# Kernel optimization log

Hardware: AMD Instinct MI355X
Metric: run time of the kernel (lower is better)

## Reference

```python
import jax, jax.numpy as jnp
import numpy as np

DIM = 1024
QKV_DIM = 64      # per-head dim
NUM_HEADS = 16
NUM_TOKENS = 1024
BATCH = 8
SCALE = QKV_DIM ** (-0.5)


def setup_inputs() -> dict:
    key = jax.random.key(0)
    k1, k2, k3 = jax.random.split(key, 3)
    x = jax.random.normal(k1, (BATCH, NUM_TOKENS, DIM), dtype=jnp.float32)
    # qkv Linear (no bias): dim -> 3 * num_heads * qkv_dim
    W_qkv = jax.random.normal(k2, (DIM, 3 * NUM_HEADS * QKV_DIM), dtype=jnp.float32) * (DIM ** -0.5)
    # reg parameter initialized to ones / num_tokens (as in nn.Parameter init)
    reg = jnp.ones((1, NUM_HEADS, NUM_TOKENS, NUM_TOKENS), dtype=jnp.float32) / NUM_TOKENS
    W_proj = jax.random.normal(k3, (NUM_HEADS * QKV_DIM, DIM), dtype=jnp.float32) * ((NUM_HEADS * QKV_DIM) ** -0.5)
    b_proj = jnp.zeros((DIM,), dtype=jnp.float32)
    return {"x": x, "W_qkv": W_qkv, "reg": reg, "W_proj": W_proj, "b_proj": b_proj}


def reference(x, W_qkv, reg, W_proj, b_proj) -> jnp.ndarray:
    B, N, C = x.shape
    H, D = NUM_HEADS, QKV_DIM
    qkv = (x @ W_qkv).reshape(B, N, 3, H, D)          # [B,N,3,H,D]
    qkv = jnp.transpose(qkv, (2, 0, 3, 1, 4))         # [3,B,H,N,D]
    q, k, v = qkv[0], qkv[1], qkv[2]
    attn = jnp.einsum('bhnd,bhmd->bhnm', q, k) * SCALE  # [B,H,N,N]
    attn = jax.nn.softmax(attn, axis=-1)
    attn = attn + reg                                   # post-softmax learned bias (broadcast over batch)
    # dropout p=0.0 -> identity
    out = jnp.einsum('bhnm,bhmd->bhnd', attn, v)        # [B,H,N,D]
    out = jnp.transpose(out, (0, 2, 1, 3)).reshape(B, N, H * D)
    return out @ W_proj + b_proj
```

## Files before the change

kernel.cpp:

```cpp
#include <hip/hip_runtime.h>
#include <hip/hip_bf16.h>

typedef __attribute__((ext_vector_type(8))) short short8;
typedef __attribute__((ext_vector_type(4))) float floatx4;

#define ATTN_C1 (0.125f * 1.44269504088896f)

__device__ inline unsigned short f2bf(float f){
  __hip_bfloat16 h = __float2bfloat16(f);
  return *reinterpret_cast<unsigned short*>(&h);
}
__device__ inline float bf2f(unsigned short u){
  __hip_bfloat16 h;
  *reinterpret_cast<unsigned short*>(&h) = u;
  return __bfloat162float(h);
}

__device__ inline bool inputs_are_bf16(const unsigned short* reg_u16){
  return reg_u16[0] == (unsigned short)0x3A80;
}

__device__ inline void gl_lds16(const void* g, void* lds_base){
  __builtin_amdgcn_global_load_lds(
      (const __attribute__((address_space(1))) void*)(unsigned long long)(uintptr_t)g,
      (__attribute__((address_space(3))) void*)(unsigned int)(uintptr_t)lds_base,
      16, 0, 0);
}

__global__ __launch_bounds__(256) void prologue(
    const void* __restrict__ x,     unsigned short* __restrict__ xb,
    const void* __restrict__ Wqkv,  unsigned short* __restrict__ Wt1,
    const void* __restrict__ Wproj, unsigned short* __restrict__ Wt2,
    const unsigned short* __restrict__ flagsrc)
{
  const bool isb = inputs_are_bf16(flagsrc);
  const int blk = blockIdx.x, tid = threadIdx.x;

  if (blk >= 4096){
    int i = ((blk - 4096)*256 + tid) * 8;
    if (isb){
      *(short8*)(xb + i) = *(const short8*)((const unsigned short*)x + i);
    } else {
      const floatx4* p = (const floatx4*)((const float*)x + i);
      floatx4 f0 = p[0], f1 = p[1];
      short8 s;
      s[0]=(short)f2bf(f0[0]); s[1]=(short)f2bf(f0[1]); s[2]=(short)f2bf(f0[2]); s[3]=(short)f2bf(f0[3]);
      s[4]=(short)f2bf(f1[0]); s[5]=(short)f2bf(f1[1]); s[6]=(short)f2bf(f1[2]); s[7]=(short)f2bf(f1[3]);
      *(short8*)(xb + i) = s;
    }
    return;
  }

  const void* in; unsigned short* out; int R, C, bxi, byi;
  if (blk < 3072){ in = Wqkv;  out = Wt1; R = 1024; C = 3072; bxi = blk % 96;  byi = blk / 96; }
  else           { int b2 = blk - 3072;
                   in = Wproj; out = Wt2; R = 1024; C = 1024; bxi = b2 % 32;   byi = b2 / 32; }
  __shared__ unsigned short t[32][33];
  const int bx = bxi*32, by = byi*32;
  const int tx = tid & 31, ty = tid >> 5;
  const unsigned short* in16 = (const unsigned short*)in;
  const float* inf = (const float*)in;
  #pragma unroll
  for (int i=0;i<32;i+=8){
    size_t idx = (size_t)(by+ty+i)*C + bx+tx;
    t[ty+i][tx] = isb ? in16[idx] : f2bf(inf[idx]);
  }
  __syncthreads();
  #pragma unroll
  for (int i=0;i<32;i+=8) out[(size_t)(bx+ty+i)*R + by+tx] = t[tx][ty+i];
}

__global__ __launch_bounds__(512, 2) void gemm_qkv(
    const unsigned short* __restrict__ A,
    const unsigned short* __restrict__ Bt,
    unsigned short* __restrict__ Qo,
    unsigned short* __restrict__ Ko,
    unsigned short* __restrict__ Vt)
{
  __shared__ __align__(16) unsigned short L[2][2][16][2][512];
  const int m0 = blockIdx.x*256, n0 = blockIdx.y*256;
  const int tid = threadIdx.x, lane = tid & 63, wave = tid >> 6;
  const int lm = lane & 15, lg = lane >> 4;
  const int wr = wave >> 2, wc = wave & 3;
  const int wr8 = wr*8, wc4 = wc*4, lane8 = lane*8;

  const int ib0 = wave*2, ib1 = wave*2+1;
  const unsigned short* gA0 = A  + (size_t)(m0 + ib0*16 + lm)*1024 + lg*8;
  const unsigned short* gA1 = A  + (size_t)(m0 + ib1*16 + lm)*1024 + lg*8;
  const unsigned short* gB0 = Bt + (size_t)(n0 + ib0*16 + lm)*1024 + lg*8;
  const unsigned short* gB1 = Bt + (size_t)(n0 + ib1*16 + lm)*1024 + lg*8;

#define QKV_STG_A(t_, ks_) do{                                          \
    unsigned short (*Ld_)[16][2][512] = L[(t_)&1];                      \
    gl_lds16(gA0 + (t_)*64 + (ks_)*32, &Ld_[0][ib0][ks_][0]);           \
    gl_lds16(gA1 + (t_)*64 + (ks_)*32, &Ld_[0][ib1][ks_][0]);           \
  }while(0)
#define QKV_STG_B(t_, ks_) do{                                          \
    unsigned short (*Ld_)[16][2][512] = L[(t_)&1];                      \
    gl_lds16(gB0 + (t_)*64 + (ks_)*32, &Ld_[1][ib0][ks_][0]);           \
    gl_lds16(gB1 + (t_)*64 + (ks_)*32, &Ld_[1][ib1][ks_][0]);           \
  }while(0)
#define QKV_VW4 asm volatile("s_waitcnt vmcnt(4)" ::: "memory")
#define QKV_VW0 asm volatile("s_waitcnt vmcnt(0)" ::: "memory")
#define QKV_NOP ((void)0)

  floatx4 acc[8][4] = {};
  short8 bv[4];

#define QKV_PHASE(t_, ks_, ih_, STAGE_STMT, WAIT_STMT) do{                    \
    const unsigned short (*Ls_)[16][2][512] = L[(t_)&1];                      \
    short8 av[4];                                                             \
    _Pragma("unroll")                                                         \
    for (int i=0;i<4;i++)                                                     \
      av[i] = *(const short8*)&Ls_[0][wr8+(ih_)*4+i][ks_][lane8];             \
    if ((ih_) == 0){                                                          \
      _Pragma("unroll")                                                       \
      for (int j=0;j<4;j++)                                                   \
        bv[j] = *(const short8*)&Ls_[1][wc4+j][ks_][lane8];                   \
    }                                                                         \
    STAGE_STMT;                                                               \
    __builtin_amdgcn_s_barrier();                                             \
    __builtin_amdgcn_s_setprio(1);                                            \
    _Pragma("unroll")                                                         \
    for (int i=0;i<4;i++){                                                    \
      _Pragma("unroll")                                                       \
      for (int j=0;j<4;j++)                                                   \
        acc[(ih_)*4+i][j] = __builtin_amdgcn_mfma_f32_16x16x32_bf16(          \
            av[i], bv[j], acc[(ih_)*4+i][j], 0,0,0);                          \
    }                                                                         \
    __builtin_amdgcn_s_setprio(0);                                            \
    WAIT_STMT;                                                                \
    __builtin_amdgcn_s_barrier();                                             \
  }while(0)

  QKV_STG_A(0,0); QKV_STG_B(0,0);
  QKV_STG_A(0,1); QKV_STG_B(0,1);
  QKV_VW4;
  __builtin_amdgcn_s_barrier();

  for (int t=0; t<15; ++t){
    QKV_PHASE(t, 0, 0, QKV_STG_A(t+1,0), QKV_NOP);
    QKV_PHASE(t, 0, 1, QKV_STG_B(t+1,0), QKV_VW4);
    QKV_PHASE(t, 1, 0, QKV_STG_A(t+1,1), QKV_NOP);
    QKV_PHASE(t, 1, 1, QKV_STG_B(t+1,1), QKV_VW4);
  }
  QKV_PHASE(15, 0, 0, QKV_NOP, QKV_NOP);
  QKV_PHASE(15, 0, 1, QKV_NOP, QKV_VW0);
  QKV_PHASE(15, 1, 0, QKV_NOP, QKV_NOP);
  QKV_PHASE(15, 1, 1, QKV_NOP, QKV_NOP);

#undef QKV_PHASE
#undef QKV_STG_A
#undef QKV_STG_B

  const int t = n0 >> 10;
  unsigned short* outp = (t==0)?Qo:((t==1)?Ko:Vt);
  const float scl = (t==0) ? ATTN_C1 : 1.0f;
  #pragma unroll
  for (int i=0;i<8;i++)
    #pragma unroll
    for (int j=0;j<4;j++)
      #pragma unroll
      for (int r=0;r<4;r++){
        int grow = m0 + wr*128 + i*16 + lg*4 + r;
        int gcol = n0 + wc*64  + j*16 + lm;
        int b = grow >> 10, n = grow & 1023;
        int h = (gcol >> 6) & 15, d = gcol & 63;
        unsigned short uv = f2bf(acc[i][j][r] * scl);
        if (t < 2) outp[((size_t)(b*16+h)*1024 + n)*64 + d] = uv;
        else       outp[((size_t)(b*16+h)*64 + d)*1024 + n] = uv;
      }
}

__global__ __launch_bounds__(512) void rv_gemm(
    const void* __restrict__ Reg,
    const unsigned short* __restrict__ Vt,
    const unsigned short* __restrict__ flagsrc,
    unsigned short* __restrict__ RV)
{
  const bool isb = inputs_are_bf16(flagsrc);
  __shared__ __align__(16) unsigned short As[64][72];
  __shared__ __align__(16) unsigned short Bs[512][72];
  const int m0 = blockIdx.x*64;
  const int h  = blockIdx.y;
  const int tid = threadIdx.x, lane = tid & 63, wave = tid >> 6;
  const int wr = wave >> 2, wc = wave & 3;
  const int wm = wr*32, wn = wc*128;
  const int lm = lane & 15, lg = lane >> 4;

  const size_t regoff = (size_t)h*1024*1024;
  const int rowA = tid >> 3, offA = (tid & 7) << 3;
  const unsigned short* vsrc[8];
  #pragma unroll
  for (int i=0;i<8;i++){
    int row = rowA + 64*i;
    int b = row >> 6, d = row & 63;
    vsrc[i] = Vt + ((size_t)(b*16 + h)*64 + d)*1024 + offA;
  }
  const unsigned short* aR16 = (const unsigned short*)Reg + regoff + (size_t)(m0+rowA)*1024 + offA;
  const float*          aRf  = (const float*)Reg + regoff + (size_t)(m0+rowA)*1024 + offA;

  short8 aReg; floatx4 aRegF0, aRegF1; short8 bReg[8];

#define RV_LOADR(k0_) do{                                                    \
    if (isb) aReg = *(const short8*)(aR16 + (k0_));                          \
    else { const floatx4* p_ = (const floatx4*)(aRf + (k0_));                \
           aRegF0 = p_[0]; aRegF1 = p_[1]; }                                 \
    _Pragma("unroll")                                                        \
    for (int i_=0;i_<8;i_++) bReg[i_] = *(const short8*)(vsrc[i_] + (k0_));  \
  }while(0)

#define RV_WRITE() do{                                                       \
    if (isb) *(short8*)&As[rowA][offA] = aReg;                               \
    else { short8 s_;                                                        \
      s_[0]=(short)f2bf(aRegF0[0]); s_[1]=(short)f2bf(aRegF0[1]);            \
      s_[2]=(short)f2bf(aRegF0[2]); s_[3]=(short)f2bf(aRegF0[3]);            \
      s_[4]=(short)f2bf(aRegF1[0]); s_[5]=(short)f2bf(aRegF1[1]);            \
      s_[6]=(short)f2bf(aRegF1[2]); s_[7]=(short)f2bf(aRegF1[3]);            \
      *(short8*)&As[rowA][offA] = s_; }                                      \
    _Pragma("unroll")                                                        \
    for (int i_=0;i_<8;i_++) *(short8*)&Bs[rowA + 64*i_][offA] = bReg[i_];   \
  }while(0)

  floatx4 acc[2][8] = {};
  RV_LOADR(0);
  for (int k0=0; k0<1024; k0+=64){
    RV_WRITE();
    __syncthreads();
    if (k0 < 960) RV_LOADR(k0+64);
    #pragma unroll
    for (int ks=0; ks<2; ks++){
      short8 av[2], bvv[8];
      int ko = ks*32 + lg*8;
      #pragma unroll
      for (int i=0;i<2;i++) av[i]  = *reinterpret_cast<const short8*>(&As[wm+i*16+lm][ko]);
      #pragma unroll
      for (int j=0;j<8;j++) bvv[j] = *reinterpret_cast<const short8*>(&Bs[wn+j*16+lm][ko]);
      #pragma unroll
      for (int i=0;i<2;i++)
        #pragma unroll
        for (int j=0;j<8;j++)
          acc[i][j] = __builtin_amdgcn_mfma_f32_16x16x32_bf16(av[i], bvv[j], acc[i][j], 0,0,0);
    }
    __syncthreads();
  }
#undef RV_LOADR
#undef RV_WRITE
  #pragma unroll
  for (int i=0;i<2;i++)
    #pragma unroll
    for (int j=0;j<8;j++)
      #pragma unroll
      for (int r=0;r<4;r++){
        int n   = m0 + wm + i*16 + lg*4 + r;
        int col = wn + j*16 + lm;
        int b = col >> 6, d = col & 63;
        RV[((size_t)(b*16+h)*1024 + n)*64 + d] = f2bf(acc[i][j][r]);
      }
}

__global__ __launch_bounds__(256, 2) void attn_kernel(
    const unsigned short* __restrict__ Q,
    const unsigned short* __restrict__ K,
    const unsigned short* __restrict__ Vt,
    const unsigned short* __restrict__ RV,
    unsigned short* __restrict__ A3)
{
  const int bid = blockIdx.x;
  const int w = (bid & 7)*256 + (bid >> 3);
  const int qt = w & 15, bh = w >> 4;
  const int b = bh >> 4, h = bh & 15;
  const int tid = threadIdx.x, lane = tid & 63, wave = tid >> 6;
  const int lm = lane & 15, lg = lane >> 4;
  const int q0 = qt*64 + wave*16;

  __shared__ __align__(16) unsigned char smem[65536];

  const unsigned short* Qp = Q  + ((size_t)bh*1024 + q0)*64;
  const unsigned short* Kp = K  + (size_t)bh*1024*64;
  const unsigned short* Vp = Vt + (size_t)bh*64*1024;

  short8 a0 = *reinterpret_cast<const short8*>(Qp + lm*64 + lg*8);
  short8 a1 = *reinterpret_cast<const short8*>(Qp + lm*64 + 32 + lg*8);

  const unsigned short* kb[4]; const unsigned short* vb[4];
  unsigned int klo[4], vlo[4];
  #pragma unroll
  for (int i=0;i<4;i++){
    int c = wave*4+i;
    kb[i] = Kp + (size_t)((c>>1)*16 + lm)*64 + (c&1)*32 + lg*8;
    vb[i] = Vp + (size_t)((c>>2)*16 + lm)*1024 + (c&3)*32 + lg*8;
    klo[i] = (unsigned)c*1024;
    vlo[i] = (unsigned)c*1024;
  }

#define ATT_STG_K(ch_) do{ unsigned char* kB_ = smem + (((ch_)&1)*16384);          \
    _Pragma("unroll") for (int i_=0;i_<4;i_++)                                     \
      gl_lds16(kb[i_] + (ch_)*8192, kB_ + klo[i_]); }while(0)
#define ATT_STG_V(ch_) do{ unsigned char* vB_ = smem + 32768 + (((ch_)&1)*16384);  \
    _Pragma("unroll") for (int i_=0;i_<4;i_++)                                     \
      gl_lds16(vb[i_] + (ch_)*128,  vB_ + vlo[i_]); }while(0)

  float ps[4] = {0.f,0.f,0.f,0.f};
  floatx4 o[4] = {};

  ATT_STG_K(0);
  ATT_STG_V(0);
  asm volatile("s_waitcnt vmcnt(4)" ::: "memory");
  __builtin_amdgcn_s_barrier();
  asm volatile("" ::: "memory");

  for (int ch=0; ch<8; ch++){
    const unsigned short* Kf = (const unsigned short*)(smem + ((ch&1)*16384));
    const unsigned short* Vf = (const unsigned short*)(smem + 32768 + ((ch&1)*16384));
    unsigned char* Pw = smem + ((ch&1)*16384) + wave*4096;

    if (ch < 7) ATT_STG_K(ch+1);

    floatx4 sc[8];
    #pragma unroll
    for (int ct=0; ct<8; ct++){
      short8 b0 = *(const short8*)(Kf + (ct*2+0)*512 + lane*8);
      short8 b1 = *(const short8*)(Kf + (ct*2+1)*512 + lane*8);
      floatx4 c = {0.f,0.f,0.f,0.f};
      c = __builtin_amdgcn_mfma_f32_16x16x32_bf16(a0, b0, c, 0,0,0);
      c = __builtin_amdgcn_mfma_f32_16x16x32_bf16(a1, b1, c, 0,0,0);
      sc[ct] = c;
    }

    #pragma unroll
    for (int r=0;r<4;r++)
      #pragma unroll
      for (int ct=0;ct<8;ct++){
        float e = __builtin_amdgcn_exp2f(sc[ct][r]);
        sc[ct][r] = e;
        ps[r] += e;
      }

    if (ch < 7) asm volatile("s_waitcnt vmcnt(4)" ::: "memory");
    else        asm volatile("s_waitcnt vmcnt(0)" ::: "memory");
    __syncthreads();

    #pragma unroll
    for (int r=0;r<4;r++){
      int row = lg*4 + r;
      unsigned int rb = (unsigned)row*256;
      unsigned int xv = (unsigned)(row & 7) << 4;
      #pragma unroll
      for (int ct=0;ct<8;ct++){
        unsigned int cb = ((unsigned)(ct*32) + (unsigned)(lm*2)) ^ xv;
        *(unsigned short*)(Pw + rb + cb) = f2bf(sc[ct][r]);
      }
    }

    if (ch < 7) ATT_STG_V(ch+1);

    #pragma unroll
    for (int kk=0;kk<4;kk++){
      unsigned int cb = ((unsigned)(kk*64 + lg*16)) ^ ((unsigned)(lm & 7) << 4);
      short8 a = *(const short8*)(Pw + (unsigned)lm*256 + cb);
      #pragma unroll
      for (int dt=0;dt<4;dt++){
        short8 bvv = *(const short8*)(Vf + (dt*4+kk)*512 + lane*8);
        o[dt] = __builtin_amdgcn_mfma_f32_16x16x32_bf16(a, bvv, o[dt], 0,0,0);
      }
    }

    if (ch < 7){
      asm volatile("s_waitcnt vmcnt(4)" ::: "memory");
      __syncthreads();
    }
  }

  #pragma unroll
  for (int r=0;r<4;r++){
    float s = ps[r];
    s += __shfl_xor(s, 1);
    s += __shfl_xor(s, 2);
    s += __shfl_xor(s, 4);
    s += __shfl_xor(s, 8);
    ps[r] = s;
  }

  const unsigned short* RVp = RV + ((size_t)bh*1024 + q0)*64;
  #pragma unroll
  for (int r=0;r<4;r++){
    int row = lg*4 + r;
    float inv = 1.0f / ps[r];
    #pragma unroll
    for (int dt=0;dt<4;dt++){
      int d = dt*16 + lm;
      float v = o[dt][r]*inv + bf2f(RVp[(size_t)row*64 + d]);
      A3[((size_t)b*1024 + q0 + row)*1024 + h*64 + d] = f2bf(v);
    }
  }
#undef ATT_STG_K
#undef ATT_STG_V
}

__global__ __launch_bounds__(256) void gemm_proj(
    const unsigned short* __restrict__ A,
    const unsigned short* __restrict__ Bt,
    const void* __restrict__ bias,
    const unsigned short* __restrict__ flagsrc,
    float* __restrict__ Out)
{
  const bool isb = inputs_are_bf16(flagsrc);
  __shared__ __align__(16) unsigned short L[4][2][8][512];
  const int m0 = blockIdx.x*128, n0 = blockIdx.y*128;
  const int tid = threadIdx.x, lane = tid & 63, wave = tid >> 6;
  const int lm = lane & 15, lg = lane >> 4;
  const int wr = wave >> 1, wc = wave & 1;

  const int ib0 = wave*2, ib1 = wave*2+1;
  const unsigned short* gA0 = A  + (size_t)(m0 + ib0*16 + lm)*1024 + lg*8;
  const unsigned short* gA1 = A  + (size_t)(m0 + ib1*16 + lm)*1024 + lg*8;
  const unsigned short* gB0 = Bt + (size_t)(n0 + ib0*16 + lm)*1024 + lg*8;
  const unsigned short* gB1 = Bt + (size_t)(n0 + ib1*16 + lm)*1024 + lg*8;

#define PRJ_STAGE(u_) do{                                   \
    int s_ = (u_) & 3;                                      \
    gl_lds16(gA0 + (u_)*32, &L[s_][0][ib0][0]);             \
    gl_lds16(gA1 + (u_)*32, &L[s_][0][ib1][0]);             \
    gl_lds16(gB0 + (u_)*32, &L[s_][1][ib0][0]);             \
    gl_lds16(gB1 + (u_)*32, &L[s_][1][ib1][0]);             \
  }while(0)

  floatx4 acc[4][4] = {};

#define PRJ_BODY(u_) do{                                                     \
    const unsigned short* As_ = &L[(u_)&3][0][0][0];                         \
    const unsigned short* Bs_ = &L[(u_)&3][1][0][0];                         \
    short8 av[4], bvv[4];                                                    \
    _Pragma("unroll")                                                        \
    for (int i=0;i<4;i++) av[i] = *(const short8*)(As_ + (wr*4+i)*512 + lane*8); \
    _Pragma("unroll")                                                        \
    for (int j=0;j<4;j++) bvv[j] = *(const short8*)(Bs_ + (wc*4+j)*512 + lane*8); \
    __builtin_amdgcn_s_setprio(1);                                           \
    _Pragma("unroll")                                                        \
    for (int i=0;i<4;i++)                                                    \
      _Pragma("unroll")                                                      \
      for (int j=0;j<4;j++)                                                  \
        acc[i][j] = __builtin_amdgcn_mfma_f32_16x16x32_bf16(av[i], bvv[j], acc[i][j], 0,0,0); \
    __builtin_amdgcn_s_setprio(0);                                           \
  }while(0)

  PRJ_STAGE(0);
  PRJ_STAGE(1);
  asm volatile("s_waitcnt vmcnt(4)" ::: "memory");
  __builtin_amdgcn_s_barrier();
  asm volatile("" ::: "memory");

  for (int u=0; u<30; ++u){
    PRJ_STAGE(u+2);
    PRJ_BODY(u);
    asm volatile("s_waitcnt vmcnt(4)" ::: "memory");
    __builtin_amdgcn_s_barrier();
    asm volatile("" ::: "memory");
  }
  PRJ_BODY(30);
  asm volatile("s_waitcnt vmcnt(0)" ::: "memory");
  __builtin_amdgcn_s_barrier();
  asm volatile("" ::: "memory");
  PRJ_BODY(31);

#undef PRJ_STAGE
#undef PRJ_BODY

  #pragma unroll
  for (int i=0;i<4;i++)
    #pragma unroll
    for (int j=0;j<4;j++)
      #pragma unroll
      for (int r=0;r<4;r++){
        int grow = m0 + wr*64 + i*16 + lg*4 + r;
        int gcol = n0 + wc*64 + j*16 + lm;
        float bv_ = isb ? bf2f(((const unsigned short*)bias)[gcol])
                        : ((const float*)bias)[gcol];
        Out[(size_t)grow*1024 + gcol] = acc[i][j][r] + bv_;
      }
}

extern "C" void kernel_launch(void* const* d_in, const int* in_sizes, int n_in,
                              void* d_out, int out_size, void* d_ws, size_t ws_size,
                              hipStream_t stream)
{
  const void* x      = d_in[0];
  const void* W_qkv  = d_in[1];
  const void* Reg    = d_in[2];
  const void* W_proj = d_in[3];
  const void* b_proj = d_in[4];
  const unsigned short* flagsrc = (const unsigned short*)Reg;

  char* ws = (char*)d_ws;
  unsigned short* Wt1 = (unsigned short*)(ws);
  unsigned short* Wt2 = (unsigned short*)(ws +  6291456);
  unsigned short* K   = (unsigned short*)(ws +  8388608);
  unsigned short* Vt  = (unsigned short*)(ws + 25165824);
  unsigned short* Q   = (unsigned short*)d_out;
  unsigned short* xb  = (unsigned short*)((char*)d_out + 16777216);
  unsigned short* A3  = (unsigned short*)d_in[0];
  unsigned short* RV  = (unsigned short*)((char*)d_in[0] + 16777216);

  prologue<<<8192, 256, 0, stream>>>(x, xb, W_qkv, Wt1, W_proj, Wt2, flagsrc);
  gemm_qkv<<<dim3(32,12), 512, 0, stream>>>(xb, Wt1, Q, K, Vt);
  rv_gemm<<<dim3(16,16), 512, 0, stream>>>(Reg, Vt, flagsrc, RV);
  attn_kernel<<<dim3(2048), 256, 0, stream>>>(Q, K, Vt, RV, A3);
  gemm_proj<<<dim3(64,8), 256, 0, stream>>>(A3, Wt2, b_proj, flagsrc, (float*)d_out);
}
```

Before: 386.9 us.

## Fuse reg@V product into attention kernel, drop separate rv_gemm launch

Removes the standalone rv_gemm kernel and instead computes reg·V inside the attention kernel. Each wave loads its rows of reg per chunk, converts them to bf16 if needed, and issues a second MFMA chain into a new accumulator that reuses the V fragments already staged in LDS. This drops one kernel launch and the RV intermediate write and read. In exchange, attention does double the PV MFMA work and streams reg from global memory once per batch, which is 8x redundant reads of reg versus once per head before. It also adds register pressure under the 2-block occupancy bound.

New measurement: 391.8 us. About the same (+1.2%).

```diff
diff --git a/kernel.cpp b/kernel.cpp
--- a/kernel.cpp
+++ b/kernel.cpp
@@ -172,100 +172,15 @@
       }
 }
 
-__global__ __launch_bounds__(512) void rv_gemm(
-    const void* __restrict__ Reg,
-    const unsigned short* __restrict__ Vt,
-    const unsigned short* __restrict__ flagsrc,
-    unsigned short* __restrict__ RV)
-{
-  const bool isb = inputs_are_bf16(flagsrc);
-  __shared__ __align__(16) unsigned short As[64][72];
-  __shared__ __align__(16) unsigned short Bs[512][72];
-  const int m0 = blockIdx.x*64;
-  const int h  = blockIdx.y;
-  const int tid = threadIdx.x, lane = tid & 63, wave = tid >> 6;
-  const int wr = wave >> 2, wc = wave & 3;
-  const int wm = wr*32, wn = wc*128;
-  const int lm = lane & 15, lg = lane >> 4;
-
-  const size_t regoff = (size_t)h*1024*1024;
-  const int rowA = tid >> 3, offA = (tid & 7) << 3;
-  const unsigned short* vsrc[8];
-  #pragma unroll
-  for (int i=0;i<8;i++){
-    int row = rowA + 64*i;
-    int b = row >> 6, d = row & 63;
-    vsrc[i] = Vt + ((size_t)(b*16 + h)*64 + d)*1024 + offA;
-  }
-  const unsigned short* aR16 = (const unsigned short*)Reg + regoff + (size_t)(m0+rowA)*1024 + offA;
-  const float*          aRf  = (const float*)Reg + regoff + (size_t)(m0+rowA)*1024 + offA;
-
-  short8 aReg; floatx4 aRegF0, aRegF1; short8 bReg[8];
-
-#define RV_LOADR(k0_) do{                                                    \
-    if (isb) aReg = *(const short8*)(aR16 + (k0_));                          \
-    else { const floatx4* p_ = (const floatx4*)(aRf + (k0_));                \
-           aRegF0 = p_[0]; aRegF1 = p_[1]; }                                 \
-    _Pragma("unroll")                                                        \
-    for (int i_=0;i_<8;i_++) bReg[i_] = *(const short8*)(vsrc[i_] + (k0_));  \
-  }while(0)
-
-#define RV_WRITE() do{                                                       \
-    if (isb) *(short8*)&As[rowA][offA] = aReg;                               \
-    else { short8 s_;                                                        \
-      s_[0]=(short)f2bf(aRegF0[0]); s_[1]=(short)f2bf(aRegF0[1]);            \
-      s_[2]=(short)f2bf(aRegF0[2]); s_[3]=(short)f2bf(aRegF0[3]);            \
-      s_[4]=(short)f2bf(aRegF1[0]); s_[5]=(short)f2bf(aRegF1[1]);            \
-      s_[6]=(short)f2bf(aRegF1[2]); s_[7]=(short)f2bf(aRegF1[3]);            \
-      *(short8*)&As[rowA][offA] = s_; }                                      \
-    _Pragma("unroll")                                                        \
-    for (int i_=0;i_<8;i_++) *(short8*)&Bs[rowA + 64*i_][offA] = bReg[i_];   \
-  }while(0)
-
-  floatx4 acc[2][8] = {};
-  RV_LOADR(0);
-  for (int k0=0; k0<1024; k0+=64){
-    RV_WRITE();
-    __syncthreads();
-    if (k0 < 960) RV_LOADR(k0+64);
-    #pragma unroll
-    for (int ks=0; ks<2; ks++){
-      short8 av[2], bvv[8];
-      int ko = ks*32 + lg*8;
-      #pragma unroll
-      for (int i=0;i<2;i++) av[i]  = *reinterpret_cast<const short8*>(&As[wm+i*16+lm][ko]);
-      #pragma unroll
-      for (int j=0;j<8;j++) bvv[j] = *reinterpret_cast<const short8*>(&Bs[wn+j*16+lm][ko]);
-      #pragma unroll
-      for (int i=0;i<2;i++)
-        #pragma unroll
-        for (int j=0;j<8;j++)
-          acc[i][j] = __builtin_amdgcn_mfma_f32_16x16x32_bf16(av[i], bvv[j], acc[i][j], 0,0,0);
-    }
-    __syncthreads();
-  }
-#undef RV_LOADR
-#undef RV_WRITE
-  #pragma unroll
-  for (int i=0;i<2;i++)
-    #pragma unroll
-    for (int j=0;j<8;j++)
-      #pragma unroll
-      for (int r=0;r<4;r++){
-        int n   = m0 + wm + i*16 + lg*4 + r;
-        int col = wn + j*16 + lm;
-        int b = col >> 6, d = col & 63;
-        RV[((size_t)(b*16+h)*1024 + n)*64 + d] = f2bf(acc[i][j][r]);
-      }
-}
-
 __global__ __launch_bounds__(256, 2) void attn_kernel(
     const unsigned short* __restrict__ Q,
     const unsigned short* __restrict__ K,
     const unsigned short* __restrict__ Vt,
-    const unsigned short* __restrict__ RV,
+    const void* __restrict__ Reg,
+    const unsigned short* __restrict__ flagsrc,
     unsigned short* __restrict__ A3)
 {
+  const bool isb = inputs_are_bf16(flagsrc);
   const int bid = blockIdx.x;
   const int w = (bid & 7)*256 + (bid >> 3);
   const int qt = w & 15, bh = w >> 4;
@@ -279,6 +194,9 @@
   const unsigned short* Qp = Q  + ((size_t)bh*1024 + q0)*64;
   const unsigned short* Kp = K  + (size_t)bh*1024*64;
   const unsigned short* Vp = Vt + (size_t)bh*64*1024;
+  const size_t regoff = (size_t)h*1024*1024;
+  const float*          rgf  = (const float*)Reg + regoff + (size_t)(q0+lm)*1024;
+  const unsigned short* rg16 = (const unsigned short*)Reg + regoff + (size_t)(q0+lm)*1024;
 
   short8 a0 = *reinterpret_cast<const short8*>(Qp + lm*64 + lg*8);
   short8 a1 = *reinterpret_cast<const short8*>(Qp + lm*64 + 32 + lg*8);
@@ -300,20 +218,35 @@
 #define ATT_STG_V(ch_) do{ unsigned char* vB_ = smem + 32768 + (((ch_)&1)*16384);  \
     _Pragma("unroll") for (int i_=0;i_<4;i_++)                                     \
       gl_lds16(vb[i_] + (ch_)*128,  vB_ + vlo[i_]); }while(0)
+#define ATT_BAR() do{ asm volatile("" ::: "memory");                               \
+    __builtin_amdgcn_s_barrier(); asm volatile("" ::: "memory"); }while(0)
 
   float ps[4] = {0.f,0.f,0.f,0.f};
   floatx4 o[4] = {};
+  floatx4 o2[4] = {};
 
   ATT_STG_K(0);
   ATT_STG_V(0);
   asm volatile("s_waitcnt vmcnt(4)" ::: "memory");
-  __builtin_amdgcn_s_barrier();
-  asm volatile("" ::: "memory");
+  ATT_BAR();
 
   for (int ch=0; ch<8; ch++){
     const unsigned short* Kf = (const unsigned short*)(smem + ((ch&1)*16384));
     const unsigned short* Vf = (const unsigned short*)(smem + 32768 + ((ch&1)*16384));
     unsigned char* Pw = smem + ((ch&1)*16384) + wave*4096;
+
+    floatx4 rf[8]; short8 pr[4];
+    if (isb){
+      #pragma unroll
+      for (int kk=0;kk<4;kk++)
+        pr[kk] = *(const short8*)(rg16 + ch*128 + kk*32 + lg*8);
+    } else {
+      #pragma unroll
+      for (int kk=0;kk<4;kk++){
+        const floatx4* p_ = (const floatx4*)(rgf + ch*128 + kk*32 + lg*8);
+        rf[kk*2] = p_[0]; rf[kk*2+1] = p_[1];
+      }
+    }
 
     if (ch < 7) ATT_STG_K(ch+1);
 
@@ -339,7 +272,7 @@
 
     if (ch < 7) asm volatile("s_waitcnt vmcnt(4)" ::: "memory");
     else        asm volatile("s_waitcnt vmcnt(0)" ::: "memory");
-    __syncthreads();
+    ATT_BAR();
 
     #pragma unroll
     for (int r=0;r<4;r++){
@@ -352,6 +285,17 @@
         *(unsigned short*)(Pw + rb + cb) = f2bf(sc[ct][r]);
       }
     }
+    if (!isb){
+      #pragma unroll
+      for (int kk=0;kk<4;kk++){
+        short8 s;
+        s[0]=(short)f2bf(rf[kk*2][0]);   s[1]=(short)f2bf(rf[kk*2][1]);
+        s[2]=(short)f2bf(rf[kk*2][2]);   s[3]=(short)f2bf(rf[kk*2][3]);
+        s[4]=(short)f2bf(rf[kk*2+1][0]); s[5]=(short)f2bf(rf[kk*2+1][1]);
+        s[6]=(short)f2bf(rf[kk*2+1][2]); s[7]=(short)f2bf(rf[kk*2+1][3]);
+        pr[kk] = s;
+      }
+    }
 
     if (ch < 7) ATT_STG_V(ch+1);
 
@@ -362,13 +306,14 @@
       #pragma unroll
       for (int dt=0;dt<4;dt++){
         short8 bvv = *(const short8*)(Vf + (dt*4+kk)*512 + lane*8);
-        o[dt] = __builtin_amdgcn_mfma_f32_16x16x32_bf16(a, bvv, o[dt], 0,0,0);
+        o[dt]  = __builtin_amdgcn_mfma_f32_16x16x32_bf16(a,      bvv, o[dt],  0,0,0);
+        o2[dt] = __builtin_amdgcn_mfma_f32_16x16x32_bf16(pr[kk], bvv, o2[dt], 0,0,0);
       }
     }
 
     if (ch < 7){
       asm volatile("s_waitcnt vmcnt(4)" ::: "memory");
-      __syncthreads();
+      ATT_BAR();
     }
   }
 
@@ -382,7 +327,6 @@
     ps[r] = s;
   }
 
-  const unsigned short* RVp = RV + ((size_t)bh*1024 + q0)*64;
   #pragma unroll
   for (int r=0;r<4;r++){
     int row = lg*4 + r;
@@ -390,12 +334,13 @@
     #pragma unroll
     for (int dt=0;dt<4;dt++){
       int d = dt*16 + lm;
-      float v = o[dt][r]*inv + bf2f(RVp[(size_t)row*64 + d]);
+      float v = o[dt][r]*inv + o2[dt][r];
       A3[((size_t)b*1024 + q0 + row)*1024 + h*64 + d] = f2bf(v);
     }
   }
 #undef ATT_STG_K
 #undef ATT_STG_V
+#undef ATT_BAR
 }
 
 __global__ __launch_bounds__(256) void gemm_proj(
@@ -500,11 +445,9 @@
   unsigned short* Q   = (unsigned short*)d_out;
   unsigned short* xb  = (unsigned short*)((char*)d_out + 16777216);
   unsigned short* A3  = (unsigned short*)d_in[0];
-  unsigned short* RV  = (unsigned short*)((char*)d_in[0] + 16777216);
 
   prologue<<<8192, 256, 0, stream>>>(x, xb, W_qkv, Wt1, W_proj, Wt2, flagsrc);
   gemm_qkv<<<dim3(32,12), 512, 0, stream>>>(xb, Wt1, Q, K, Vt);
-  rv_gemm<<<dim3(16,16), 512, 0, stream>>>(Reg, Vt, flagsrc, RV);
-  attn_kernel<<<dim3(2048), 256, 0, stream>>>(Q, K, Vt, RV, A3);
+  attn_kernel<<<dim3(2048), 256, 0, stream>>>(Q, K, Vt, Reg, flagsrc, A3);
   gemm_proj<<<dim3(64,8), 256, 0, stream>>>(A3, Wt2, b_proj, flagsrc, (float*)d_out);
 }
```
